# Optimization experiments

Hardware: AMD Instinct MI355X
Metric: run time of the kernel (lower is better)

Reference implementation:

```python
import jax, jax.numpy as jnp
import numpy as np

VOCAB, EMB, ENC = 100000, 256, 256
N_INTENTS, N_SLOTS, LEN_INTENT = 64, 128, 64
B, S = 64, 128


def setup_inputs() -> dict:
    key = jax.random.key(0)
    ks = jax.random.split(key, 8)
    sc = 0.02
    return {
        "token_ids": jax.random.randint(ks[0], (B, S), 0, VOCAB),
        "all_intents": jax.random.randint(ks[1], (B,), 0, N_INTENTS),
        "emb_table": jax.random.normal(ks[2], (VOCAB, EMB), jnp.float32) * sc,
        "doc_enc_W": jax.random.normal(ks[3], (EMB, ENC), jnp.float32) * sc,
        "doc_enc_b": jnp.zeros((ENC,), jnp.float32),
        "slot_enc_W": jax.random.normal(ks[4], (EMB, ENC), jnp.float32) * sc,
        "slot_enc_b": jnp.zeros((ENC,), jnp.float32),
        "doc_dec_W": jax.random.normal(ks[5], (ENC, N_INTENTS), jnp.float32) * sc,
        "doc_dec_b": jnp.zeros((N_INTENTS,), jnp.float32),
        "slot_dec_W": jax.random.normal(ks[6], (ENC + LEN_INTENT, N_SLOTS), jnp.float32) * sc,
        "slot_dec_b": jnp.zeros((N_SLOTS,), jnp.float32),
    }


def reference(token_ids, all_intents, emb_table, doc_enc_W, doc_enc_b,
              slot_enc_W, slot_enc_b, doc_dec_W, doc_dec_b,
              slot_dec_W, slot_dec_b):
    # word embedding lookup: [B, S, EMB] (memory-bound gather)
    emb = emb_table[token_ids]
    # doc encoder: pool sentence then project (batched stand-in for the
    # per-sentence python loop in the original encode())
    sent = jnp.mean(emb, axis=1)                                    # [B, EMB]
    sent_enc = jax.nn.relu(sent @ doc_enc_W + doc_enc_b)            # [B, ENC]
    # intent logits (doc_decoder applied per sentence)
    intent_batch = sent_enc @ doc_dec_W + doc_dec_b                 # [B, N_INTENTS]
    # slot encoder: per-word projection (batched stand-in for per-word loop)
    word_enc = jax.nn.relu(jnp.einsum('bse,eh->bsh', emb, slot_enc_W) + slot_enc_b)
    # use_intent: one-hot of given intent appended to every word encoding
    add_feats = jax.nn.one_hot(all_intents, LEN_INTENT, dtype=word_enc.dtype)  # [B, LEN_INTENT]
    add_feats = jnp.broadcast_to(add_feats[:, None, :], (B, S, LEN_INTENT))
    slot_in = jnp.concatenate([word_enc, add_feats], axis=-1)       # [B, S, ENC+LEN_INTENT]
    slots = jnp.einsum('bsh,ho->bso', slot_in, slot_dec_W) + slot_dec_b
    slots_batch = slots.reshape(B * S, N_SLOTS)  # torch.cat along dim 0 over words
    return intent_batch, slots_batch
```

## Files before the change

kernel.cpp:

```cpp
#include <hip/hip_runtime.h>
#include <hip/hip_bf16.h>

typedef __attribute__((ext_vector_type(8))) short bf16x8;
typedef __attribute__((ext_vector_type(4))) float f32x4;

#define BATCH 64
#define SEQ   128
#define EMB   256
#define ENC   256
#define NIN   64
#define NSL   128

static __device__ __forceinline__ bf16x8 cvt8(const float4 lo, const float4 hi) {
    union { bf16x8 v; __hip_bfloat16 h[8]; } u;
    u.h[0] = __float2bfloat16(lo.x); u.h[1] = __float2bfloat16(lo.y);
    u.h[2] = __float2bfloat16(lo.z); u.h[3] = __float2bfloat16(lo.w);
    u.h[4] = __float2bfloat16(hi.x); u.h[5] = __float2bfloat16(hi.y);
    u.h[6] = __float2bfloat16(hi.z); u.h[7] = __float2bfloat16(hi.w);
    return u.v;
}

static __device__ __forceinline__ bf16x8 load_bT(const float* __restrict__ W,
                                                 int ldn, int k0, int n) {
    union { bf16x8 v; __hip_bfloat16 h[8]; } u;
    #pragma unroll
    for (int j = 0; j < 8; ++j)
        u.h[j] = __float2bfloat16(W[(long)(k0 + j) * ldn + n]);
    return u.v;
}

__global__ __launch_bounds__(256) void fused_kernel(
    const int*   __restrict__ token_ids,
    const int*   __restrict__ all_intents,
    const float* __restrict__ emb_table,
    const float* __restrict__ doc_enc_W,
    const float* __restrict__ doc_enc_b,
    const float* __restrict__ slot_enc_W,
    const float* __restrict__ slot_enc_b,
    const float* __restrict__ doc_dec_W,
    const float* __restrict__ doc_dec_b,
    const float* __restrict__ slot_dec_W,
    const float* __restrict__ slot_dec_b,
    float* __restrict__ out_intent,
    float* __restrict__ out_slots)
{
    __shared__ __align__(16) __hip_bfloat16 lds_we[32 * 264];
    __shared__ __align__(16) float red[4][256];
    __shared__ float sent[ENC];
    __shared__ float senc[ENC];

    const int blk = blockIdx.x;

    if (blk < 256) {
        const int row0 = blk * 32;
        const int wave = threadIdx.x >> 6;
        const int lane = threadIdx.x & 63;
        const int l16  = lane & 15;
        const int quad = lane >> 4;

        f32x4 acc[2][4];
        #pragma unroll
        for (int mt = 0; mt < 2; ++mt)
            #pragma unroll
            for (int nt = 0; nt < 4; ++nt)
                acc[mt][nt] = (f32x4){0.f, 0.f, 0.f, 0.f};

        const long tok0 = token_ids[row0 + l16];
        const long tok1 = token_ids[row0 + 16 + l16];
        const float* arow0 = emb_table + tok0 * EMB + quad * 8;
        const float* arow1 = emb_table + tok1 * EMB + quad * 8;
        const int nbase1 = wave * 64;

        #pragma unroll
        for (int ks = 0; ks < 8; ++ks) {
            const bf16x8 a0 = cvt8(*(const float4*)(arow0 + ks * 32),
                                   *(const float4*)(arow0 + ks * 32 + 4));
            const bf16x8 a1 = cvt8(*(const float4*)(arow1 + ks * 32),
                                   *(const float4*)(arow1 + ks * 32 + 4));
            const int k0 = ks * 32 + quad * 8;
            #pragma unroll
            for (int nt = 0; nt < 4; ++nt) {
                const bf16x8 bf = load_bT(slot_enc_W, ENC, k0, nbase1 + nt * 16 + l16);
                acc[0][nt] = __builtin_amdgcn_mfma_f32_16x16x32_bf16(a0, bf, acc[0][nt], 0, 0, 0);
                acc[1][nt] = __builtin_amdgcn_mfma_f32_16x16x32_bf16(a1, bf, acc[1][nt], 0, 0, 0);
            }
        }

        #pragma unroll
        for (int nt = 0; nt < 4; ++nt) {
            const int col = nbase1 + nt * 16 + l16;
            const float bias = slot_enc_b[col];
            #pragma unroll
            for (int mt = 0; mt < 2; ++mt) {
                #pragma unroll
                for (int r = 0; r < 4; ++r) {
                    const int row = mt * 16 + quad * 4 + r;
                    lds_we[row * 264 + col] =
                        __float2bfloat16(fmaxf(acc[mt][nt][r] + bias, 0.f));
                }
            }
        }
        __syncthreads();

        f32x4 acc2[2][2];
        #pragma unroll
        for (int mt = 0; mt < 2; ++mt)
            #pragma unroll
            for (int nt = 0; nt < 2; ++nt)
                acc2[mt][nt] = (f32x4){0.f, 0.f, 0.f, 0.f};

        const int nbase2 = wave * 32;
        #pragma unroll
        for (int ks = 0; ks < 8; ++ks) {
            const bf16x8 a0 = *(const bf16x8*)(lds_we + l16 * 264 + ks * 32 + quad * 8);
            const bf16x8 a1 = *(const bf16x8*)(lds_we + (16 + l16) * 264 + ks * 32 + quad * 8);
            const int k0 = ks * 32 + quad * 8;
            #pragma unroll
            for (int nt = 0; nt < 2; ++nt) {
                const bf16x8 bf = load_bT(slot_dec_W, NSL, k0, nbase2 + nt * 16 + l16);
                acc2[0][nt] = __builtin_amdgcn_mfma_f32_16x16x32_bf16(a0, bf, acc2[0][nt], 0, 0, 0);
                acc2[1][nt] = __builtin_amdgcn_mfma_f32_16x16x32_bf16(a1, bf, acc2[1][nt], 0, 0, 0);
            }
        }

        const int intent = all_intents[row0 >> 7];
        const float* hotrow = slot_dec_W + (long)(256 + intent) * NSL;

        #pragma unroll
        for (int nt = 0; nt < 2; ++nt) {
            const int col = nbase2 + nt * 16 + l16;
            const float add = slot_dec_b[col] + hotrow[col];
            #pragma unroll
            for (int mt = 0; mt < 2; ++mt) {
                #pragma unroll
                for (int r = 0; r < 4; ++r) {
                    const int row = mt * 16 + quad * 4 + r;
                    out_slots[(long)(row0 + row) * NSL + col] = acc2[mt][nt][r] + add;
                }
            }
        }
    } else {
        const int b  = blk - 256;
        const int t  = threadIdx.x;
        const int wv = t >> 6;
        const int ln = t & 63;
        const int* toks = token_ids + b * SEQ;

        float4 accv = make_float4(0.f, 0.f, 0.f, 0.f);
        #pragma unroll 8
        for (int i = 0; i < 32; ++i) {
            const long tok = toks[wv * 32 + i];
            const float4 v = *(const float4*)(emb_table + tok * EMB + ln * 4);
            accv.x += v.x; accv.y += v.y; accv.z += v.z; accv.w += v.w;
        }
        *(float4*)(&red[wv][ln * 4]) = accv;
        __syncthreads();

        sent[t] = (red[0][t] + red[1][t] + red[2][t] + red[3][t]) * (1.0f / 128.0f);
        __syncthreads();

        float a = doc_enc_b[t];
        #pragma unroll 16
        for (int k = 0; k < EMB; ++k)
            a = fmaf(sent[k], doc_enc_W[k * ENC + t], a);
        senc[t] = fmaxf(a, 0.f);
        __syncthreads();

        if (t < NIN) {
            float a2 = doc_dec_b[t];
            #pragma unroll 16
            for (int k = 0; k < ENC; ++k)
                a2 = fmaf(senc[k], doc_dec_W[k * NIN + t], a2);
            out_intent[b * NIN + t] = a2;
        }
    }
}

extern "C" void kernel_launch(void* const* d_in, const int* in_sizes, int n_in,
                              void* d_out, int out_size, void* d_ws, size_t ws_size,
                              hipStream_t stream) {
    const int*   token_ids   = (const int*)d_in[0];
    const int*   all_intents = (const int*)d_in[1];
    const float* emb_table   = (const float*)d_in[2];
    const float* doc_enc_W   = (const float*)d_in[3];
    const float* doc_enc_b   = (const float*)d_in[4];
    const float* slot_enc_W  = (const float*)d_in[5];
    const float* slot_enc_b  = (const float*)d_in[6];
    const float* doc_dec_W   = (const float*)d_in[7];
    const float* doc_dec_b   = (const float*)d_in[8];
    const float* slot_dec_W  = (const float*)d_in[9];
    const float* slot_dec_b  = (const float*)d_in[10];

    float* out = (float*)d_out;

    fused_kernel<<<320, 256, 0, stream>>>(
        token_ids, all_intents, emb_table, doc_enc_W, doc_enc_b,
        slot_enc_W, slot_enc_b, doc_dec_W, doc_dec_b, slot_dec_W, slot_dec_b,
        out, out + BATCH * NIN);
}
```

Measured before the change: 173.0 us.

## Prepack weights to bf16 MFMA layout and stage embeddings in LDS

```diff
diff --git a/kernel.cpp b/kernel.cpp
--- a/kernel.cpp
+++ b/kernel.cpp
@@ -11,22 +11,34 @@
 #define NIN   64
 #define NSL   128
 
-static __device__ __forceinline__ bf16x8 cvt8(const float4 lo, const float4 hi) {
-    union { bf16x8 v; __hip_bfloat16 h[8]; } u;
-    u.h[0] = __float2bfloat16(lo.x); u.h[1] = __float2bfloat16(lo.y);
-    u.h[2] = __float2bfloat16(lo.z); u.h[3] = __float2bfloat16(lo.w);
-    u.h[4] = __float2bfloat16(hi.x); u.h[5] = __float2bfloat16(hi.y);
-    u.h[6] = __float2bfloat16(hi.z); u.h[7] = __float2bfloat16(hi.w);
-    return u.v;
-}
-
-static __device__ __forceinline__ bf16x8 load_bT(const float* __restrict__ W,
-                                                 int ldn, int k0, int n) {
-    union { bf16x8 v; __hip_bfloat16 h[8]; } u;
-    #pragma unroll
-    for (int j = 0; j < 8; ++j)
-        u.h[j] = __float2bfloat16(W[(long)(k0 + j) * ldn + n]);
-    return u.v;
+#define W1P_ELEMS (32 * 256 * 8)
+#define W2P_ELEMS (32 * 128 * 8)
+
+__global__ __launch_bounds__(256) void prep_kernel(
+    const float* __restrict__ slot_enc_W,
+    const float* __restrict__ slot_dec_W,
+    __hip_bfloat16* __restrict__ w1p,
+    __hip_bfloat16* __restrict__ w2p)
+{
+    const int tid = blockIdx.x * 256 + threadIdx.x;
+    if (tid < 8192) {
+        const int n  = tid & 255;
+        const int bk = tid >> 8;
+        union { bf16x8 v; __hip_bfloat16 h[8]; } u;
+        #pragma unroll
+        for (int j = 0; j < 8; ++j)
+            u.h[j] = __float2bfloat16(slot_enc_W[(bk * 8 + j) * ENC + n]);
+        *(bf16x8*)(w1p + (size_t)tid * 8) = u.v;
+    } else {
+        const int t2 = tid - 8192;
+        const int n  = t2 & 127;
+        const int bk = t2 >> 7;
+        union { bf16x8 v; __hip_bfloat16 h[8]; } u;
+        #pragma unroll
+        for (int j = 0; j < 8; ++j)
+            u.h[j] = __float2bfloat16(slot_dec_W[(bk * 8 + j) * NSL + n]);
+        *(bf16x8*)(w2p + (size_t)t2 * 8) = u.v;
+    }
 }
 
 __global__ __launch_bounds__(256) void fused_kernel(
@@ -35,54 +47,59 @@
     const float* __restrict__ emb_table,
     const float* __restrict__ doc_enc_W,
     const float* __restrict__ doc_enc_b,
-    const float* __restrict__ slot_enc_W,
     const float* __restrict__ slot_enc_b,
     const float* __restrict__ doc_dec_W,
     const float* __restrict__ doc_dec_b,
     const float* __restrict__ slot_dec_W,
     const float* __restrict__ slot_dec_b,
+    const __hip_bfloat16* __restrict__ w1p,
+    const __hip_bfloat16* __restrict__ w2p,
     float* __restrict__ out_intent,
     float* __restrict__ out_slots)
 {
-    __shared__ __align__(16) __hip_bfloat16 lds_we[32 * 264];
-    __shared__ __align__(16) float red[4][256];
-    __shared__ float sent[ENC];
-    __shared__ float senc[ENC];
+    __shared__ __align__(16) char smem[2 * 16 * 264 * 2];
 
     const int blk = blockIdx.x;
 
-    if (blk < 256) {
-        const int row0 = blk * 32;
+    if (blk < 512) {
+        __hip_bfloat16* lds_emb = (__hip_bfloat16*)smem;
+        __hip_bfloat16* lds_we  = (__hip_bfloat16*)(smem + 16 * 264 * 2);
+
+        const int row0 = blk * 16;
         const int wave = threadIdx.x >> 6;
         const int lane = threadIdx.x & 63;
         const int l16  = lane & 15;
         const int quad = lane >> 4;
 
-        f32x4 acc[2][4];
-        #pragma unroll
-        for (int mt = 0; mt < 2; ++mt)
-            #pragma unroll
-            for (int nt = 0; nt < 4; ++nt)
-                acc[mt][nt] = (f32x4){0.f, 0.f, 0.f, 0.f};
-
-        const long tok0 = token_ids[row0 + l16];
-        const long tok1 = token_ids[row0 + 16 + l16];
-        const float* arow0 = emb_table + tok0 * EMB + quad * 8;
-        const float* arow1 = emb_table + tok1 * EMB + quad * 8;
+        #pragma unroll
+        for (int i = 0; i < 4; ++i) {
+            const int idx = i * 256 + threadIdx.x;
+            const int r   = idx >> 6;
+            const int c4  = idx & 63;
+            const long tok = token_ids[row0 + r];
+            const float4 v = *(const float4*)(emb_table + tok * EMB + c4 * 4);
+            union { ushort4 s; __hip_bfloat16 h[4]; } u;
+            u.h[0] = __float2bfloat16(v.x); u.h[1] = __float2bfloat16(v.y);
+            u.h[2] = __float2bfloat16(v.z); u.h[3] = __float2bfloat16(v.w);
+            *(ushort4*)(lds_emb + r * 264 + c4 * 4) = u.s;
+        }
+        __syncthreads();
+
+        f32x4 acc[4];
+        #pragma unroll
+        for (int nt = 0; nt < 4; ++nt)
+            acc[nt] = (f32x4){0.f, 0.f, 0.f, 0.f};
+
         const int nbase1 = wave * 64;
-
         #pragma unroll
         for (int ks = 0; ks < 8; ++ks) {
-            const bf16x8 a0 = cvt8(*(const float4*)(arow0 + ks * 32),
-                                   *(const float4*)(arow0 + ks * 32 + 4));
-            const bf16x8 a1 = cvt8(*(const float4*)(arow1 + ks * 32),
-                                   *(const float4*)(arow1 + ks * 32 + 4));
-            const int k0 = ks * 32 + quad * 8;
+            const bf16x8 a0 = *(const bf16x8*)(lds_emb + l16 * 264 + ks * 32 + quad * 8);
+            const int kblk = ks * 4 + quad;
             #pragma unroll
             for (int nt = 0; nt < 4; ++nt) {
-                const bf16x8 bf = load_bT(slot_enc_W, ENC, k0, nbase1 + nt * 16 + l16);
-                acc[0][nt] = __builtin_amdgcn_mfma_f32_16x16x32_bf16(a0, bf, acc[0][nt], 0, 0, 0);
-                acc[1][nt] = __builtin_amdgcn_mfma_f32_16x16x32_bf16(a1, bf, acc[1][nt], 0, 0, 0);
+                const int n = nbase1 + nt * 16 + l16;
+                const bf16x8 bf = *(const bf16x8*)(w1p + ((size_t)kblk * 256 + n) * 8);
+                acc[nt] = __builtin_amdgcn_mfma_f32_16x16x32_bf16(a0, bf, acc[nt], 0, 0, 0);
             }
         }
 
@@ -91,39 +108,33 @@
             const int col = nbase1 + nt * 16 + l16;
             const float bias = slot_enc_b[col];
             #pragma unroll
-            for (int mt = 0; mt < 2; ++mt) {
-                #pragma unroll
-                for (int r = 0; r < 4; ++r) {
-                    const int row = mt * 16 + quad * 4 + r;
-                    lds_we[row * 264 + col] =
-                        __float2bfloat16(fmaxf(acc[mt][nt][r] + bias, 0.f));
-                }
-            }
-        }
-        __syncthreads();
-
-        f32x4 acc2[2][2];
-        #pragma unroll
-        for (int mt = 0; mt < 2; ++mt)
-            #pragma unroll
-            for (int nt = 0; nt < 2; ++nt)
-                acc2[mt][nt] = (f32x4){0.f, 0.f, 0.f, 0.f};
+            for (int r = 0; r < 4; ++r) {
+                const int row = quad * 4 + r;
+                lds_we[row * 264 + col] =
+                    __float2bfloat16(fmaxf(acc[nt][r] + bias, 0.f));
+            }
+        }
+        __syncthreads();
+
+        f32x4 acc2[2];
+        #pragma unroll
+        for (int nt = 0; nt < 2; ++nt)
+            acc2[nt] = (f32x4){0.f, 0.f, 0.f, 0.f};
 
         const int nbase2 = wave * 32;
         #pragma unroll
         for (int ks = 0; ks < 8; ++ks) {
             const bf16x8 a0 = *(const bf16x8*)(lds_we + l16 * 264 + ks * 32 + quad * 8);
-            const bf16x8 a1 = *(const bf16x8*)(lds_we + (16 + l16) * 264 + ks * 32 + quad * 8);
-            const int k0 = ks * 32 + quad * 8;
+            const int kblk = ks * 4 + quad;
             #pragma unroll
             for (int nt = 0; nt < 2; ++nt) {
-                const bf16x8 bf = load_bT(slot_dec_W, NSL, k0, nbase2 + nt * 16 + l16);
-                acc2[0][nt] = __builtin_amdgcn_mfma_f32_16x16x32_bf16(a0, bf, acc2[0][nt], 0, 0, 0);
-                acc2[1][nt] = __builtin_amdgcn_mfma_f32_16x16x32_bf16(a1, bf, acc2[1][nt], 0, 0, 0);
-            }
-        }
-
-        const int intent = all_intents[row0 >> 7];
+                const int n = nbase2 + nt * 16 + l16;
+                const bf16x8 bf = *(const bf16x8*)(w2p + ((size_t)kblk * 128 + n) * 8);
+                acc2[nt] = __builtin_amdgcn_mfma_f32_16x16x32_bf16(a0, bf, acc2[nt], 0, 0, 0);
+            }
+        }
+
+        const int intent = all_intents[blk >> 3];
         const float* hotrow = slot_dec_W + (long)(256 + intent) * NSL;
 
         #pragma unroll
@@ -131,16 +142,17 @@
             const int col = nbase2 + nt * 16 + l16;
             const float add = slot_dec_b[col] + hotrow[col];
             #pragma unroll
-            for (int mt = 0; mt < 2; ++mt) {
-                #pragma unroll
-                for (int r = 0; r < 4; ++r) {
-                    const int row = mt * 16 + quad * 4 + r;
-                    out_slots[(long)(row0 + row) * NSL + col] = acc2[mt][nt][r] + add;
-                }
+            for (int r = 0; r < 4; ++r) {
+                const int row = quad * 4 + r;
+                out_slots[(long)(row0 + row) * NSL + col] = acc2[nt][r] + add;
             }
         }
     } else {
-        const int b  = blk - 256;
+        float* red  = (float*)smem;
+        float* sent = (float*)(smem + 4096);
+        float* senc = (float*)(smem + 4096 + 1024);
+
+        const int b  = blk - 512;
         const int t  = threadIdx.x;
         const int wv = t >> 6;
         const int ln = t & 63;
@@ -153,10 +165,11 @@
             const float4 v = *(const float4*)(emb_table + tok * EMB + ln * 4);
             accv.x += v.x; accv.y += v.y; accv.z += v.z; accv.w += v.w;
         }
-        *(float4*)(&red[wv][ln * 4]) = accv;
-        __syncthreads();
-
-        sent[t] = (red[0][t] + red[1][t] + red[2][t] + red[3][t]) * (1.0f / 128.0f);
+        *(float4*)(&red[wv * 256 + ln * 4]) = accv;
+        __syncthreads();
+
+        sent[t] = (red[0 * 256 + t] + red[1 * 256 + t] +
+                   red[2 * 256 + t] + red[3 * 256 + t]) * (1.0f / 128.0f);
         __syncthreads();
 
         float a = doc_enc_b[t];
@@ -191,10 +204,16 @@
     const float* slot_dec_W  = (const float*)d_in[9];
     const float* slot_dec_b  = (const float*)d_in[10];
 
+    __hip_bfloat16* w1p = (__hip_bfloat16*)d_ws;
+    __hip_bfloat16* w2p = w1p + W1P_ELEMS;
+
     float* out = (float*)d_out;
 
-    fused_kernel<<<320, 256, 0, stream>>>(
+    prep_kernel<<<48, 256, 0, stream>>>(slot_enc_W, slot_dec_W, w1p, w2p);
+
+    fused_kernel<<<576, 256, 0, stream>>>(
         token_ids, all_intents, emb_table, doc_enc_W, doc_enc_b,
-        slot_enc_W, slot_enc_b, doc_dec_W, doc_dec_b, slot_dec_W, slot_dec_b,
+        slot_enc_b, doc_dec_W, doc_dec_b, slot_dec_W, slot_dec_b,
+        w1p, w2p,
         out, out + BATCH * NIN);
 }
```

Result: faster. 169.5 us (-2.0%).
